# Kernel optimization log

Hardware: AMD Instinct MI355X
Metric: run time of the kernel (lower is better)

Reference implementation:

```python
import jax, jax.numpy as jnp
import numpy as np

B, T_PREFIX, C_IN = 8, 6144, 8
OUT_LEN, OUT_C = 2048, 8
AUX_DIM = 16
D_MODEL, D_STATE, HEADDIM, EXPAND = 256, 32, 64, 2
D_INNER = EXPAND * D_MODEL            # 512
NHEADS = D_INNER // HEADDIM           # 8
CONV_DIM = D_INNER + 2 * D_STATE      # 576
D_PROJ = 2 * D_INNER + 2 * D_STATE + NHEADS  # 1096
N_LAYERS = 2
CHUNK = 64
PATCH = 16
PRECONV_K = 5
DCONV_K = 4


def setup_inputs() -> dict:
    key = jax.random.key(0)
    ks = iter(jax.random.split(key, 64))
    def rn(shape, s=0.02):
        return s * jax.random.normal(next(ks), shape, jnp.float32)
    inp = dict(
        x_prefix=jax.random.normal(next(ks), (B, T_PREFIX, C_IN), jnp.float32),
        y_aux=jax.random.normal(next(ks), (B, AUX_DIM), jnp.float32),
        pre_conv_w=rn((D_MODEL, C_IN, PRECONV_K), 0.1),
        pre_conv_b=rn((D_MODEL,)),
        patch_w=rn((D_MODEL, D_MODEL, PATCH), 0.05),
        patch_b=rn((D_MODEL,)),
        mask_token=rn((D_MODEL,)),
        aux_w=rn((AUX_DIM, D_MODEL), 0.1),
        aux_b=rn((D_MODEL,)),
        patch_out_w=rn((2 * D_MODEL, OUT_C * PATCH), 0.05),
        patch_out_b=rn((OUT_C * PATCH,)),
    )
    for d in ('fwd', 'bwd'):
        inp[f'{d}_norm_w'] = jnp.ones((N_LAYERS, D_MODEL), jnp.float32)
        inp[f'{d}_inproj'] = rn((N_LAYERS, D_MODEL, D_PROJ), 0.05)
        inp[f'{d}_conv_w'] = rn((N_LAYERS, CONV_DIM, DCONV_K), 0.2)
        inp[f'{d}_conv_b'] = rn((N_LAYERS, CONV_DIM))
        inp[f'{d}_dtbias'] = rn((N_LAYERS, NHEADS), 0.5)
        inp[f'{d}_Alog'] = jnp.tile(jnp.log(jnp.arange(1, NHEADS + 1, dtype=jnp.float32)), (N_LAYERS, 1))
        inp[f'{d}_D'] = jnp.ones((N_LAYERS, NHEADS), jnp.float32)
        inp[f'{d}_gnorm'] = jnp.ones((N_LAYERS, D_INNER), jnp.float32)
        inp[f'{d}_outproj'] = rn((N_LAYERS, D_INNER, D_MODEL), 0.05)
    return inp


def rmsnorm(x, w, eps=1e-5):
    return x * jax.lax.rsqrt(jnp.mean(x * x, axis=-1, keepdims=True) + eps) * w


def conv1d(x, w, b, stride, pad):  # x: [B,C,T], w: [O,I,K]
    y = jax.lax.conv_general_dilated(x, w, (stride,), [(pad, pad)],
                                     dimension_numbers=('NCH', 'OIH', 'NCH'))
    return y + b[None, :, None]


def mamba_block(u, inproj, conv_w, conv_b, dtbias, Alog, Dp, gnorm_w, outproj):
    # Mamba-2/SSD style block: in_proj -> z | xBC | dt, causal depthwise conv,
    # selective scan with per-head scalar decay A, +D skip, gated RMSNorm, out_proj.
    b, T, _ = u.shape
    zxbcdt = u @ inproj                                   # [b,T,D_PROJ]
    z = zxbcdt[..., :D_INNER]
    xBC = zxbcdt[..., D_INNER:D_INNER + CONV_DIM]
    dt = jax.nn.softplus(zxbcdt[..., -NHEADS:] + dtbias)  # [b,T,H]
    # causal depthwise conv over time
    xc = jax.lax.conv_general_dilated(xBC.transpose(0, 2, 1), conv_w[:, None, :], (1,),
                                      [(DCONV_K - 1, 0)],
                                      dimension_numbers=('NCH', 'OIH', 'NCH'),
                                      feature_group_count=CONV_DIM)
    xBC = jax.nn.silu((xc + conv_b[None, :, None]).transpose(0, 2, 1))
    xs = xBC[..., :D_INNER].reshape(b, T, NHEADS, HEADDIM)  # [b,T,H,P]
    Bm = xBC[..., D_INNER:D_INNER + D_STATE]                # [b,T,N]
    Cm = xBC[..., D_INNER + D_STATE:]                       # [b,T,N]
    A = -jnp.exp(Alog)                                      # [H]

    def step(h, inps):  # h: [b,H,P,N]
        dt_t, x_t, B_t, C_t = inps
        dA = jnp.exp(dt_t * A)[:, :, None, None]
        h = h * dA + (dt_t[:, :, None] * x_t)[..., None] * B_t[:, None, None, :]
        y = jnp.einsum('bhpn,bn->bhp', h, C_t)
        return h, y

    h0 = jnp.zeros((b, NHEADS, HEADDIM, D_STATE), u.dtype)
    _, ys = jax.lax.scan(step, h0, (dt.transpose(1, 0, 2), xs.transpose(1, 0, 2, 3),
                                    Bm.transpose(1, 0, 2), Cm.transpose(1, 0, 2)))
    y = ys.transpose(1, 0, 2, 3) + Dp[None, None, :, None] * xs
    y = y.reshape(b, T, D_INNER)
    y = rmsnorm(y * jax.nn.silu(z), gnorm_w)
    return y @ outproj


def reference(x_prefix, y_aux, pre_conv_w, pre_conv_b, patch_w, patch_b, mask_token,
              aux_w, aux_b, fwd_norm_w, fwd_inproj, fwd_conv_w, fwd_conv_b, fwd_dtbias,
              fwd_Alog, fwd_D, fwd_gnorm, fwd_outproj, bwd_norm_w, bwd_inproj,
              bwd_conv_w, bwd_conv_b, bwd_dtbias, bwd_Alog, bwd_D, bwd_gnorm,
              bwd_outproj, patch_out_w, patch_out_b):
    b = x_prefix.shape[0]
    t_total = T_PREFIX + OUT_LEN
    x_full = jnp.pad(x_prefix, ((0, 0), (0, OUT_LEN), (0, 0)))        # zeros for future
    x = jax.nn.silu(conv1d(x_full.transpose(0, 2, 1), pre_conv_w, pre_conv_b, 1, PRECONV_K // 2))
    x = conv1d(x, patch_w, patch_b, PATCH, 0).transpose(0, 2, 1)      # [b, n_tokens, d_model]
    n_tokens = x.shape[1]
    # eval mode: deterministic future-patch mask, dropout is identity
    starts = jnp.arange(n_tokens) * PATCH
    mask = (starts >= T_PREFIX)[None, :, None]
    x = jnp.where(mask, mask_token[None, None, :], x)
    aux_bias = jax.nn.silu(y_aux @ aux_w + aux_b)[:, None, :]
    x = x + aux_bias
    pad_t = (-n_tokens) % CHUNK
    if pad_t:
        x = jnp.pad(x, ((0, 0), (0, pad_t), (0, 0)))
    h_f = x
    h_b = x[:, ::-1]
    for i in range(N_LAYERS):
        h_f = h_f + mamba_block(rmsnorm(h_f, fwd_norm_w[i]), fwd_inproj[i], fwd_conv_w[i],
                                fwd_conv_b[i], fwd_dtbias[i], fwd_Alog[i], fwd_D[i],
                                fwd_gnorm[i], fwd_outproj[i])
        h_b = h_b + mamba_block(rmsnorm(h_b, bwd_norm_w[i]), bwd_inproj[i], bwd_conv_w[i],
                                bwd_conv_b[i], bwd_dtbias[i], bwd_Alog[i], bwd_D[i],
                                bwd_gnorm[i], bwd_outproj[i])
    h = jnp.concatenate([h_f, h_b[:, ::-1]], axis=-1)[:, :n_tokens]   # [b,n,2*d_model]
    patch_pred = h @ patch_out_w + patch_out_b                        # [b,n,out_c*patch]
    y = patch_pred.reshape(b, n_tokens, OUT_C, PATCH).reshape(b, n_tokens * PATCH, OUT_C)
    y = y[:, :t_total, :]
    return y[:, T_PREFIX:, :]
```

## Files before the change

kernel.cpp:

```cpp
#include <hip/hip_runtime.h>
#include <hip/hip_bf16.h>
#include <math.h>

#define BSZ      8
#define TPREF    6144
#define CIN      8
#define DMODEL   256
#define DINNER   512
#define DSTATE   32
#define NHEADS   8
#define HEADDIM  64
#define CONVDIM  576
#define DPROJ    1096
#define NTOK     512
#define NVIS     384
#define TBWD     128
#define MFWD     (BSZ * NTOK)
#define MBWD     (BSZ * TBWD)
#define MALL     (MFWD + MBWD)

typedef float f32x4 __attribute__((ext_vector_type(4)));
typedef __bf16 bf16x8 __attribute__((ext_vector_type(8)));

__device__ __forceinline__ float silu_f(float x) { return x / (1.f + expf(-x)); }

#define ASYNC16(gp, lp) \
    __builtin_amdgcn_global_load_lds((const __attribute__((address_space(1))) void*)(gp), \
                                     (__attribute__((address_space(3))) void*)(lp), 16, 0, 0)

__global__ __launch_bounds__(256) void gemm_mfma(
    const __bf16* __restrict__ A, const __bf16* __restrict__ Bt,
    float* __restrict__ C, const float* __restrict__ bias,
    int N, int K, int ldc, int flags, long pstr) {
    __shared__ char sm[16384];
    int tid = threadIdx.x;
    int m0 = blockIdx.y * 128, n0 = blockIdx.x * 128;
    int klen = K / gridDim.z;
    int kbeg = blockIdx.z * klen;
    int w = tid >> 6, l = tid & 63;
    int wm = w >> 1, wn = w & 1;
    int lm = l & 15, q = l >> 4;

    f32x4 acc[4][4];
    #pragma unroll
    for (int i = 0; i < 4; i++)
        #pragma unroll
        for (int j = 0; j < 4; j++) acc[i][j] = (f32x4)0.f;

    for (int k0 = 0; k0 < klen; k0 += 32) {
        int kb = kbeg + k0;
        #pragma unroll
        for (int i = 0; i < 2; i++) {
            int s = i * 256 + tid;
            ASYNC16(A + (size_t)(m0 + (s >> 2)) * K + kb + (s & 3) * 8, sm + s * 16);
        }
        #pragma unroll
        for (int i = 0; i < 2; i++) {
            int s = i * 256 + tid;
            ASYNC16(Bt + (size_t)(n0 + (s >> 2)) * K + kb + (s & 3) * 8, sm + 8192 + s * 16);
        }
        __syncthreads();
        bf16x8 af[4], bfr[4];
        #pragma unroll
        for (int mf = 0; mf < 4; mf++)
            af[mf] = *(const bf16x8*)(sm + (wm * 64 + mf * 16 + lm) * 64 + q * 16);
        #pragma unroll
        for (int nf = 0; nf < 4; nf++)
            bfr[nf] = *(const bf16x8*)(sm + 8192 + (wn * 64 + nf * 16 + lm) * 64 + q * 16);
        #pragma unroll
        for (int mf = 0; mf < 4; mf++)
            #pragma unroll
            for (int nf = 0; nf < 4; nf++)
                acc[mf][nf] = __builtin_amdgcn_mfma_f32_16x16x32_bf16(af[mf], bfr[nf], acc[mf][nf], 0, 0, 0);
        __syncthreads();
    }

    #pragma unroll
    for (int mf = 0; mf < 4; mf++) {
        int mbase = m0 + wm * 64 + mf * 16 + q * 4;
        #pragma unroll
        for (int nf = 0; nf < 4; nf++) {
            int n = n0 + wn * 64 + nf * 16 + lm;
            if (n < N) {
                #pragma unroll
                for (int r = 0; r < 4; r++) {
                    float v = acc[mf][nf][r];
                    size_t ci = (size_t)(mbase + r) * ldc + n;
                    if (flags & 4) {
                        v = silu_f(v + bias[n]);
                        ((__bf16*)C)[ci] = (__bf16)v;
                    } else if (flags & 8) {
                        C[ci + (size_t)blockIdx.z * pstr] = v;
                    } else if (flags & 2) {
                        atomicAdd(C + ci, v);
                    } else {
                        C[ci] = v;
                    }
                }
            }
        }
    }
}

__global__ __launch_bounds__(256) void gemm_inproj_norm(
    const float* __restrict__ h, const float* __restrict__ wnf, const float* __restrict__ wnb,
    const __bf16* __restrict__ ipTf, const __bf16* __restrict__ ipTb,
    float* __restrict__ C) {
    __shared__ __bf16 Asm[128][264];
    __shared__ char Bsm[8192];
    int tid = threadIdx.x;
    int m0 = blockIdx.y * 128, n0 = blockIdx.x * 128;
    int dir = (m0 >= MFWD);
    const float* wnorm = dir ? wnb : wnf;
    const __bf16* Bt = dir ? ipTb : ipTf;
    {
        int row = tid >> 1, half = tid & 1;
        const float4* xr = (const float4*)(h + (size_t)(m0 + row) * 256 + half * 128);
        const float4* wr = (const float4*)(wnorm + half * 128);
        float ss = 0.f;
        #pragma unroll
        for (int c = 0; c < 32; c++) {
            float4 v = xr[c], wv = wr[c];
            ss += v.x * v.x + v.y * v.y + v.z * v.z + v.w * v.w;
            __bf16 t4b[4] = {(__bf16)(v.x * wv.x), (__bf16)(v.y * wv.y),
                             (__bf16)(v.z * wv.z), (__bf16)(v.w * wv.w)};
            *(uint2*)&Asm[row][half * 128 + c * 4] = *(uint2*)t4b;
        }
        ss += __shfl_xor(ss, 1);
        float rs = rsqrtf(ss * (1.f / 256.f) + 1e-5f);
        #pragma unroll
        for (int c = 0; c < 16; c++) {
            union { uint4 u; __bf16 hh[8]; } a;
            a.u = *(uint4*)&Asm[row][half * 128 + c * 8];
            #pragma unroll
            for (int j = 0; j < 8; j++) a.hh[j] = (__bf16)((float)a.hh[j] * rs);
            *(uint4*)&Asm[row][half * 128 + c * 8] = a.u;
        }
    }
    __syncthreads();
    int w = tid >> 6, l = tid & 63;
    int wm = w >> 1, wn_ = w & 1, lm = l & 15, q = l >> 4;
    f32x4 acc[4][4];
    #pragma unroll
    for (int i = 0; i < 4; i++)
        #pragma unroll
        for (int j = 0; j < 4; j++) acc[i][j] = (f32x4)0.f;
    for (int k0 = 0; k0 < 256; k0 += 32) {
        #pragma unroll
        for (int i = 0; i < 2; i++) {
            int s = i * 256 + tid;
            ASYNC16(Bt + (size_t)(n0 + (s >> 2)) * 256 + k0 + (s & 3) * 8, Bsm + s * 16);
        }
        __syncthreads();
        bf16x8 af[4], bfr[4];
        #pragma unroll
        for (int mf = 0; mf < 4; mf++)
            af[mf] = *(const bf16x8*)&Asm[wm * 64 + mf * 16 + lm][k0 + q * 8];
        #pragma unroll
        for (int nf = 0; nf < 4; nf++)
            bfr[nf] = *(const bf16x8*)(Bsm + (wn_ * 64 + nf * 16 + lm) * 64 + q * 16);
        #pragma unroll
        for (int mf = 0; mf < 4; mf++)
            #pragma unroll
            for (int nf = 0; nf < 4; nf++)
                acc[mf][nf] = __builtin_amdgcn_mfma_f32_16x16x32_bf16(af[mf], bfr[nf], acc[mf][nf], 0, 0, 0);
        __syncthreads();
    }
    #pragma unroll
    for (int mf = 0; mf < 4; mf++) {
        int mbase = m0 + wm * 64 + mf * 16 + q * 4;
        #pragma unroll
        for (int nf = 0; nf < 4; nf++) {
            int n = n0 + wn_ * 64 + nf * 16 + lm;
            if (n < DPROJ) {
                #pragma unroll
                for (int r = 0; r < 4; r++)
                    C[(size_t)(mbase + r) * DPROJ + n] = acc[mf][nf][r];
            }
        }
    }
}

__global__ __launch_bounds__(256) void gemm_outproj_gated(
    const __bf16* __restrict__ ysD, const float* __restrict__ zx,
    const float* __restrict__ gwf, const float* __restrict__ gwb,
    const __bf16* __restrict__ opTf, const __bf16* __restrict__ opTb,
    float* __restrict__ C) {
    __shared__ __bf16 Asm[64][520];
    __shared__ char Bsm[8192];
    int tid = threadIdx.x;
    int m0 = blockIdx.y * 64, n0 = blockIdx.x * 128;
    int dir = (m0 >= MFWD);
    const float* gw = dir ? gwb : gwf;
    const __bf16* Bt = dir ? opTb : opTf;
    {
        int row = tid >> 2, part = tid & 3;
        size_t gm = m0 + row;
        const uint4* yr = (const uint4*)(ysD + gm * 512 + part * 128);
        const float4* zr = (const float4*)(zx + gm * DPROJ + part * 128);
        const float4* gr = (const float4*)(gw + part * 128);
        float ss = 0.f;
        #pragma unroll
        for (int c = 0; c < 16; c++) {
            union { uint4 u; __bf16 hh[8]; } yv; yv.u = yr[c];
            float4 z0 = zr[c * 2], z1 = zr[c * 2 + 1];
            float4 g0 = gr[c * 2], g1 = gr[c * 2 + 1];
            float gg[8];
            gg[0] = (float)yv.hh[0] * silu_f(z0.x);
            gg[1] = (float)yv.hh[1] * silu_f(z0.y);
            gg[2] = (float)yv.hh[2] * silu_f(z0.z);
            gg[3] = (float)yv.hh[3] * silu_f(z0.w);
            gg[4] = (float)yv.hh[4] * silu_f(z1.x);
            gg[5] = (float)yv.hh[5] * silu_f(z1.y);
            gg[6] = (float)yv.hh[6] * silu_f(z1.z);
            gg[7] = (float)yv.hh[7] * silu_f(z1.w);
            #pragma unroll
            for (int j = 0; j < 8; j++) ss += gg[j] * gg[j];
            union { uint4 u; __bf16 hh[8]; } d;
            d.hh[0] = (__bf16)(gg[0] * g0.x); d.hh[1] = (__bf16)(gg[1] * g0.y);
            d.hh[2] = (__bf16)(gg[2] * g0.z); d.hh[3] = (__bf16)(gg[3] * g0.w);
            d.hh[4] = (__bf16)(gg[4] * g1.x); d.hh[5] = (__bf16)(gg[5] * g1.y);
            d.hh[6] = (__bf16)(gg[6] * g1.z); d.hh[7] = (__bf16)(gg[7] * g1.w);
            *(uint4*)&Asm[row][part * 128 + c * 8] = d.u;
        }
        ss += __shfl_xor(ss, 1);
        ss += __shfl_xor(ss, 2);
        float rs = rsqrtf(ss * (1.f / 512.f) + 1e-5f);
        #pragma unroll
        for (int c = 0; c < 16; c++) {
            union { uint4 u; __bf16 hh[8]; } a;
            a.u = *(uint4*)&Asm[row][part * 128 + c * 8];
            #pragma unroll
            for (int j = 0; j < 8; j++) a.hh[j] = (__bf16)((float)a.hh[j] * rs);
            *(uint4*)&Asm[row][part * 128 + c * 8] = a.u;
        }
    }
    __syncthreads();
    int w = tid >> 6, l = tid & 63;
    int wm = w >> 1, wn_ = w & 1, lm = l & 15, q = l >> 4;
    f32x4 acc[2][4];
    #pragma unroll
    for (int i = 0; i < 2; i++)
        #pragma unroll
        for (int j = 0; j < 4; j++) acc[i][j] = (f32x4)0.f;
    for (int k0 = 0; k0 < 512; k0 += 32) {
        #pragma unroll
        for (int i = 0; i < 2; i++) {
            int s = i * 256 + tid;
            ASYNC16(Bt + (size_t)(n0 + (s >> 2)) * 512 + k0 + (s & 3) * 8, Bsm + s * 16);
        }
        __syncthreads();
        bf16x8 af[2], bfr[4];
        #pragma unroll
        for (int mf = 0; mf < 2; mf++)
            af[mf] = *(const bf16x8*)&Asm[wm * 32 + mf * 16 + lm][k0 + q * 8];
        #pragma unroll
        for (int nf = 0; nf < 4; nf++)
            bfr[nf] = *(const bf16x8*)(Bsm + (wn_ * 64 + nf * 16 + lm) * 64 + q * 16);
        #pragma unroll
        for (int mf = 0; mf < 2; mf++)
            #pragma unroll
            for (int nf = 0; nf < 4; nf++)
                acc[mf][nf] = __builtin_amdgcn_mfma_f32_16x16x32_bf16(af[mf], bfr[nf], acc[mf][nf], 0, 0, 0);
        __syncthreads();
    }
    #pragma unroll
    for (int mf = 0; mf < 2; mf++) {
        int mbase = m0 + wm * 32 + mf * 16 + q * 4;
        #pragma unroll
        for (int nf = 0; nf < 4; nf++) {
            int n = n0 + wn_ * 64 + nf * 16 + lm;
            #pragma unroll
            for (int r = 0; r < 4; r++) {
                size_t ci = (size_t)(mbase + r) * DMODEL + n;
                C[ci] += acc[mf][nf][r];
            }
        }
    }
}

__global__ void prep_all(const float* __restrict__ pre_conv_w, const float* __restrict__ patch_w,
                         const float* __restrict__ ip0, const float* __restrict__ ip1,
                         const float* __restrict__ op0, const float* __restrict__ op1,
                         const float* __restrict__ pow_, const float* __restrict__ pob,
                         const float* __restrict__ y_aux, const float* __restrict__ aux_w,
                         const float* __restrict__ aux_b, const float* __restrict__ xp,
                         __bf16* __restrict__ WpreT, __bf16* __restrict__ WtT,
                         __bf16* __restrict__ inprojT, __bf16* __restrict__ outprojT,
                         __bf16* __restrict__ poT, float* __restrict__ auxb,
                         float* __restrict__ dout, __bf16* __restrict__ Aim) {
    __shared__ float tile[32][33];
    int bx = blockIdx.x, tid = threadIdx.x;
    int tx = tid & 31, ty = tid >> 5;
    if (bx < 256) {
        int o = bx, c = tid;
        float f[16];
        const float4* s = (const float4*)(patch_w + (size_t)o * 4096 + c * 16);
        #pragma unroll
        for (int j = 0; j < 4; j++) *(float4*)&f[j * 4] = s[j];
        #pragma unroll
        for (int k = 0; k < 16; k++)
            WtT[(size_t)o * 4096 + k * 256 + c] = (__bf16)f[k];
        return;
    }
    bx -= 256;
    if (bx < 1152) {
        int seg = bx / 288, rem = bx % 288;
        int n0 = (rem / 8) * 32, k0 = (rem % 8) * 32;
        const float* src = (seg < 2 ? ip0 : ip1) + (size_t)(seg & 1) * 256 * DPROJ;
        #pragma unroll
        for (int j = 0; j < 4; j++) {
            int r = ty + j * 8;
            int n = n0 + tx;
            tile[r][tx] = (n < DPROJ) ? src[(size_t)(k0 + r) * DPROJ + n] : 0.f;
        }
        __syncthreads();
        __bf16* dst = inprojT + (size_t)seg * 1152 * 256;
        #pragma unroll
        for (int j = 0; j < 4; j++) {
            int r = ty + j * 8;
            dst[(size_t)(n0 + r) * 256 + k0 + tx] = (__bf16)tile[tx][r];
        }
        return;
    }
    bx -= 1152;
    if (bx < 512) {
        int s = bx / 128, rem = bx % 128;
        int n0 = (rem / 16) * 32, k0 = (rem % 16) * 32;
        const float* src = (s < 2 ? op0 : op1) + (size_t)(s & 1) * DINNER * DMODEL;
        #pragma unroll
        for (int j = 0; j < 4; j++) {
            int r = ty + j * 8;
            tile[r][tx] = src[(size_t)(k0 + r) * 256 + n0 + tx];
        }
        __syncthreads();
        __bf16* dst = outprojT + (size_t)s * 256 * 512;
        #pragma unroll
        for (int j = 0; j < 4; j++) {
            int r = ty + j * 8;
            dst[(size_t)(n0 + r) * 512 + k0 + tx] = (__bf16)tile[tx][r];
        }
        return;
    }
    bx -= 512;
    if (bx < 64) {
        int n0 = (bx / 16) * 32, k0 = (bx % 16) * 32;
        #pragma unroll
        for (int j = 0; j < 4; j++) {
            int r = ty + j * 8;
            tile[r][tx] = pow_[(size_t)(k0 + r) * 128 + n0 + tx];
        }
        __syncthreads();
        #pragma unroll
        for (int j = 0; j < 4; j++) {
            int r = ty + j * 8;
            poT[(size_t)(n0 + r) * 512 + k0 + tx] = (__bf16)tile[tx][r];
        }
        return;
    }
    bx -= 64;
    if (bx < 64) {
        int idx = bx * 256 + tid;
        int o = idx >> 6, kk = idx & 63;
        WpreT[idx] = (kk < 40) ? (__bf16)pre_conv_w[o * 40 + kk] : (__bf16)0.f;
        return;
    }
    bx -= 64;
    if (bx < 512) {
        int idx = bx * 256 + tid;
        dout[idx] = pob[idx & 127];
        return;
    }
    bx -= 512;
    if (bx < 192) {
        int m = bx * 256 + tid;
        int t = m % TPREF, b = m / TPREF;
        __bf16 d[64];
        #pragma unroll
        for (int k = 0; k < 5; k++) {
            int tt = t - 2 + k;
            bool ok = (tt >= 0) && (tt < TPREF);
            const float* s = xp + ((size_t)b * TPREF + tt) * 8;
            #pragma unroll
            for (int i = 0; i < 8; i++)
                d[i * 5 + k] = ok ? (__bf16)s[i] : (__bf16)0.f;
        }
        #pragma unroll
        for (int j = 40; j < 64; j++) d[j] = (__bf16)0.f;
        uint4* o = (uint4*)(Aim + (size_t)m * 64);
        #pragma unroll
        for (int k = 0; k < 8; k++) o[k] = ((const uint4*)d)[k];
        return;
    }
    bx -= 192;
    {
        int b = bx, o = tid;
        float acc = aux_b[o];
        #pragma unroll
        for (int i = 0; i < 16; i++) acc += y_aux[b * 16 + i] * aux_w[i * 256 + o];
        auxb[b * 256 + o] = silu_f(acc);
    }
}

__global__ void assemble_kernel(const float* __restrict__ Cp4, const float* __restrict__ pb,
                                const float* __restrict__ mtok, const float* __restrict__ aux,
                                float* __restrict__ h_all) {
    int idx = blockIdx.x * 256 + threadIdx.x;
    if (idx >= BSZ * NTOK * DMODEL) return;
    int o = idx & 255, tok = (idx >> 8) & 511, b = idx >> 17;
    float v;
    if (tok < NVIS) {
        size_t ci = (size_t)(b * NVIS + tok) * 256 + o;
        v = pb[o] + Cp4[ci] + Cp4[ci + (size_t)3072 * 256] +
            Cp4[ci + (size_t)2 * 3072 * 256] + Cp4[ci + (size_t)3 * 3072 * 256];
    } else {
        v = mtok[o];
    }
    v += aux[b * 256 + o];
    h_all[idx] = v;
    if (tok >= NVIS)
        h_all[(size_t)MFWD * 256 + (size_t)(b * TBWD + (NTOK - 1 - tok)) * 256 + o] = v;
}

__global__ __launch_bounds__(256) void dwconv2_kernel(
    const float* __restrict__ zx, const float* __restrict__ cwf, const float* __restrict__ cbf,
    const float* __restrict__ cwb, const float* __restrict__ cbb,
    __bf16* __restrict__ XtF, __bf16* __restrict__ XtB,
    __bf16* __restrict__ BCF, __bf16* __restrict__ BCB) {
    int cg = blockIdx.x;
    int id = blockIdx.y;
    int b, t0, T; size_t rowbase;
    const float *cw, *cb; __bf16 *Xt, *BC;
    if (id < 64) { b = id >> 3; t0 = (id & 7) * 64; T = NTOK; rowbase = (size_t)b * NTOK;
                   cw = cwf; cb = cbf; Xt = XtF; BC = BCF; }
    else { int i2 = id - 64; b = i2 >> 1; t0 = (i2 & 1) * 64; T = TBWD;
           rowbase = (size_t)MFWD + (size_t)b * TBWD; cw = cwb; cb = cbb; Xt = XtB; BC = BCB; }
    int c0 = cg * 64;
    __shared__ float xs[67][65];
    int lane = threadIdx.x & 63, grp = threadIdx.x >> 6;
    for (int r = grp; r < 67; r += 4) {
        int t = t0 - 3 + r;
        xs[r][lane] = (t >= 0) ? zx[(rowbase + t) * DPROJ + DINNER + c0 + lane] : 0.f;
    }
    __syncthreads();
    if (cg < 8) {
        int t = lane;
        #pragma unroll
        for (int ci = grp; ci < 64; ci += 4) {
            int c = c0 + ci;
            float acc = cb[c];
            #pragma unroll
            for (int k = 0; k < 4; k++) acc += cw[c * 4 + k] * xs[t + k][ci];
            Xt[((size_t)((b * 8 + cg) * 64 + ci)) * T + t0 + t] = (__bf16)silu_f(acc);
        }
    } else {
        int c = lane;
        #pragma unroll
        for (int ti = grp; ti < 64; ti += 4) {
            float acc = cb[c0 + c];
            #pragma unroll
            for (int k = 0; k < 4; k++) acc += cw[(c0 + c) * 4 + k] * xs[ti + k][c];
            BC[((size_t)(b * T + t0 + ti)) * 64 + c] = (__bf16)silu_f(acc);
        }
    }
}

__global__ __launch_bounds__(64) void scan_local(
    const __bf16* __restrict__ XtF, const __bf16* __restrict__ XtB,
    const __bf16* __restrict__ BCF, const __bf16* __restrict__ BCB,
    const float* __restrict__ zx,
    const float* __restrict__ dtbf, const float* __restrict__ dtbb,
    const float* __restrict__ Alogf, const float* __restrict__ Alogb,
    const float* __restrict__ Dpf, const float* __restrict__ Dpb,
    __bf16* __restrict__ ysD,
    __bf16* __restrict__ ChatF, __bf16* __restrict__ ChatB,
    float* __restrict__ dSF, float* __restrict__ dSB,
    float* __restrict__ DcsF, float* __restrict__ DcsB) {
    int id = blockIdx.x, hd = blockIdx.y;
    int b, c, T, NC; size_t rowbase;
    const __bf16 *Xt, *BC; __bf16* Chat; float *dS, *Dcs;
    const float *dtb, *Alog, *Dp;
    if (id < 64) { b = id >> 3; c = id & 7; T = NTOK; NC = 8; rowbase = (size_t)b * NTOK;
                   Xt = XtF; BC = BCF; Chat = ChatF; dS = dSF; Dcs = DcsF;
                   dtb = dtbf; Alog = Alogf; Dp = Dpf; }
    else { int i2 = id - 64; b = i2 >> 1; c = i2 & 1; T = TBWD; NC = 2;
           rowbase = (size_t)MFWD + (size_t)b * TBWD;
           Xt = XtB; BC = BCB; Chat = ChatB; dS = dSB; Dcs = DcsB;
           dtb = dtbb; Alog = Alogb; Dp = Dpb; }
    int bh = b * 8 + hd;
    int t0 = c * 64;
    int lane = threadIdx.x;
    int lm = lane & 15, q = lane >> 4;
    float A = -expf(Alog[hd]);
    float Dh = Dp[hd];

    __shared__ __bf16 Xl[64][72];
    __shared__ __bf16 BCl[64][72];
    __shared__ __bf16 Pl[64][72];
    __shared__ __bf16 Wbl[32][72];
    __shared__ float lcs[64], dts[64];

    const uint4* xg = (const uint4*)(Xt + (size_t)(bh * 64 + lane) * T + t0);
    const uint4* bg = (const uint4*)(BC + ((size_t)(b * T + t0 + lane)) * 64);
    uint4 xv[8], bv[8];
    #pragma unroll
    for (int k = 0; k < 8; k++) { xv[k] = xg[k]; bv[k] = bg[k]; }
    float xdt = zx[(rowbase + t0 + lane) * DPROJ + 1088 + hd] + dtb[hd];
    float dtv = (xdt > 20.f) ? xdt : log1pf(expf(xdt));
    #pragma unroll
    for (int k = 0; k < 8; k++) {
        *(uint4*)&Xl[lane][k * 8] = xv[k];
        *(uint4*)&BCl[lane][k * 8] = bv[k];
    }
    float lc = A * dtv;
    #pragma unroll
    for (int off = 1; off < 64; off <<= 1) {
        float o = __shfl_up(lc, off);
        if (lane >= off) lc += o;
    }
    lcs[lane] = lc; dts[lane] = dtv;
    float lc63 = __shfl(lc, 63);
    float wj = expf(lc63 - lc) * dtv;
    float eli = expf(lc);
    float Dc = expf(lc63);
    if (lane == 0) Dcs[bh * NC + c] = Dc;
    {
        __bf16* co = Chat + ((size_t)(bh * NC + c) * 64 + lane) * 32;
        #pragma unroll
        for (int k = 0; k < 4; k++) {
            union { uint4 u; __bf16 h[8]; } s; s.u = bv[4 + k];
            union { uint4 u; __bf16 h[8]; } d;
            #pragma unroll
            for (int j = 0; j < 8; j++) d.h[j] = (__bf16)(eli * (float)s.h[j]);
            *(uint4*)(co + k * 8) = d.u;
        }
    }
    #pragma unroll
    for (int k = 0; k < 4; k++) {
        union { uint4 u; __bf16 h[8]; } s; s.u = bv[k];
        #pragma unroll
        for (int j = 0; j < 8; j++) Wbl[k * 8 + j][lane] = (__bf16)(wj * (float)s.h[j]);
    }
    __syncthreads();

    bf16x8 cfr[4], bfr[4];
    #pragma unroll
    for (int t4 = 0; t4 < 4; t4++) {
        cfr[t4] = *(const bf16x8*)&BCl[t4 * 16 + lm][32 + q * 8];
        bfr[t4] = *(const bf16x8*)&BCl[t4 * 16 + lm][q * 8];
    }
    #pragma unroll
    for (int ti = 0; ti < 4; ti++) {
        float lci[4];
        #pragma unroll
        for (int r = 0; r < 4; r++) lci[r] = lcs[ti * 16 + q * 4 + r];
        #pragma unroll
        for (int tj = 0; tj < 4; tj++) {
            if (tj > ti) {
                #pragma unroll
                for (int r = 0; r < 4; r++) Pl[ti * 16 + q * 4 + r][tj * 16 + lm] = (__bf16)0.f;
                continue;
            }
            f32x4 g = __builtin_amdgcn_mfma_f32_16x16x32_bf16(cfr[ti], bfr[tj], (f32x4)0.f, 0, 0, 0);
            int j = tj * 16 + lm;
            float lcj = lcs[j], dtj = dts[j];
            #pragma unroll
            for (int r = 0; r < 4; r++) {
                int i = ti * 16 + q * 4 + r;
                float v = (j <= i) ? g[r] * expf(lci[r] - lcj) * dtj : 0.f;
                if (j == i) v += Dh;
                Pl[i][j] = (__bf16)v;
            }
        }
    }
    __syncthreads();

    bf16x8 pf0[4], pf1[4], xf0[4], xf1[4];
    #pragma unroll
    for (int t4 = 0; t4 < 4; t4++) {
        pf0[t4] = *(const bf16x8*)&Pl[t4 * 16 + lm][q * 8];
        pf1[t4] = *(const bf16x8*)&Pl[t4 * 16 + lm][32 + q * 8];
        xf0[t4] = *(const bf16x8*)&Xl[t4 * 16 + lm][q * 8];
        xf1[t4] = *(const bf16x8*)&Xl[t4 * 16 + lm][32 + q * 8];
    }
    #pragma unroll
    for (int ti = 0; ti < 4; ti++) {
        #pragma unroll
        for (int tp = 0; tp < 4; tp++) {
            f32x4 y = __builtin_amdgcn_mfma_f32_16x16x32_bf16(pf0[ti], xf0[tp], (f32x4)0.f, 0, 0, 0);
            y = __builtin_amdgcn_mfma_f32_16x16x32_bf16(pf1[ti], xf1[tp], y, 0, 0, 0);
            #pragma unroll
            for (int r = 0; r < 4; r++) {
                int i = ti * 16 + q * 4 + r;
                ysD[(rowbase + t0 + i) * DINNER + hd * 64 + tp * 16 + lm] = (__bf16)y[r];
            }
        }
    }
    bf16x8 wf0[2], wf1[2];
    #pragma unroll
    for (int tn = 0; tn < 2; tn++) {
        wf0[tn] = *(const bf16x8*)&Wbl[tn * 16 + lm][q * 8];
        wf1[tn] = *(const bf16x8*)&Wbl[tn * 16 + lm][32 + q * 8];
    }
    float* dso = dS + (size_t)(bh * NC + c) * 2048;
    #pragma unroll
    for (int tp = 0; tp < 4; tp++) {
        #pragma unroll
        for (int tn = 0; tn < 2; tn++) {
            f32x4 s = __builtin_amdgcn_mfma_f32_16x16x32_bf16(xf0[tp], wf0[tn], (f32x4)0.f, 0, 0, 0);
            s = __builtin_amdgcn_mfma_f32_16x16x32_bf16(xf1[tp], wf1[tn], s, 0, 0, 0);
            #pragma unroll
            for (int r = 0; r < 4; r++) {
                int pp = tp * 16 + q * 4 + r, nn = tn * 16 + lm;
                dso[pp * 32 + nn] = s[r];
            }
        }
    }
}

__global__ __launch_bounds__(256) void scan_tail(
    const float* __restrict__ dSF, const float* __restrict__ dSB,
    const float* __restrict__ DcsF, const float* __restrict__ DcsB,
    const __bf16* __restrict__ ChatF, const __bf16* __restrict__ ChatB,
    __bf16* __restrict__ ysD) {
    int blk = blockIdx.x;
    int dir = blk >= 64;
    int bh = blk & 63;
    int NC = dir ? 2 : 8;
    int T = dir ? TBWD : NTOK;
    int b = bh >> 3, hd = bh & 7;
    size_t rowbase = dir ? ((size_t)MFWD + (size_t)b * TBWD) : ((size_t)b * NTOK);
    const float* dS = dir ? dSB : dSF;
    const float* Dcs = dir ? DcsB : DcsF;
    const __bf16* Chat = dir ? ChatB : ChatF;
    int tid = threadIdx.x;
    __shared__ __bf16 Spl[8][64][40];
    {
        int p = tid >> 2, n0 = (tid & 3) * 8;
        float S[8];
        #pragma unroll
        for (int j = 0; j < 8; j++) S[j] = 0.f;
        for (int c = 0; c < NC; c++) {
            union { uint4 u; __bf16 hh[8]; } o;
            #pragma unroll
            for (int j = 0; j < 8; j++) o.hh[j] = (__bf16)S[j];
            *(uint4*)&Spl[c][p][n0] = o.u;
            float Dc = Dcs[bh * NC + c];
            const float4* dp = (const float4*)(dS + ((size_t)(bh * NC + c)) * 2048 + tid * 8);
            float4 d0 = dp[0], d1 = dp[1];
            S[0] = Dc * S[0] + d0.x; S[1] = Dc * S[1] + d0.y;
            S[2] = Dc * S[2] + d0.z; S[3] = Dc * S[3] + d0.w;
            S[4] = Dc * S[4] + d1.x; S[5] = Dc * S[5] + d1.y;
            S[6] = Dc * S[6] + d1.z; S[7] = Dc * S[7] + d1.w;
        }
    }
    __syncthreads();
    int w = tid >> 6, l = tid & 63, lm = l & 15, q = l >> 4;
    for (int c = 1 + w; c < NC; c += 4) {
        int t0 = c * 64;
        const __bf16* Cb = Chat + (size_t)(bh * NC + c) * 2048;
        bf16x8 cf[4], sf[4];
        #pragma unroll
        for (int t4 = 0; t4 < 4; t4++) {
            cf[t4] = *(const bf16x8*)(Cb + (t4 * 16 + lm) * 32 + q * 8);
            sf[t4] = *(const bf16x8*)&Spl[c][t4 * 16 + lm][q * 8];
        }
        #pragma unroll
        for (int ti = 0; ti < 4; ti++) {
            #pragma unroll
            for (int tp = 0; tp < 4; tp++) {
                f32x4 y = __builtin_amdgcn_mfma_f32_16x16x32_bf16(cf[ti], sf[tp], (f32x4)0.f, 0, 0, 0);
                #pragma unroll
                for (int r = 0; r < 4; r++) {
                    int i = ti * 16 + q * 4 + r;
                    size_t idx = (rowbase + t0 + i) * DINNER + hd * 64 + tp * 16 + lm;
                    ysD[idx] = (__bf16)((float)ysD[idx] + y[r]);
                }
            }
        }
    }
}

__global__ void hcat_kernel(const float* __restrict__ h_all, __bf16* __restrict__ hc) {
    int idx = blockIdx.x * 256 + threadIdx.x;
    if (idx >= BSZ * TBWD * DINNER) return;
    int c = idx & 511, j = (idx >> 9) & 127, b = idx >> 16;
    float v = (c < 256) ? h_all[(size_t)(b * NTOK + NVIS + j) * 256 + c]
                        : h_all[(size_t)MFWD * 256 + (size_t)(b * TBWD + (TBWD - 1 - j)) * 256 + (c - 256)];
    hc[idx] = (__bf16)v;
}

extern "C" void kernel_launch(void* const* d_in, const int* in_sizes, int n_in,
                              void* d_out, int out_size, void* d_ws, size_t ws_size,
                              hipStream_t stream) {
    const float* x_prefix    = (const float*)d_in[0];
    const float* y_aux       = (const float*)d_in[1];
    const float* pre_conv_w  = (const float*)d_in[2];
    const float* pre_conv_b  = (const float*)d_in[3];
    const float* patch_w     = (const float*)d_in[4];
    const float* patch_b     = (const float*)d_in[5];
    const float* mask_token  = (const float*)d_in[6];
    const float* aux_w       = (const float*)d_in[7];
    const float* aux_b       = (const float*)d_in[8];
    const float* patch_out_w = (const float*)d_in[9];
    const float* patch_out_b = (const float*)d_in[10];
    const float* w_norm[2]   = {(const float*)d_in[11], (const float*)d_in[20]};
    const float* w_inproj[2] = {(const float*)d_in[12], (const float*)d_in[21]};
    const float* w_convw[2]  = {(const float*)d_in[13], (const float*)d_in[22]};
    const float* w_convb[2]  = {(const float*)d_in[14], (const float*)d_in[23]};
    const float* w_dtb[2]    = {(const float*)d_in[15], (const float*)d_in[24]};
    const float* w_alog[2]   = {(const float*)d_in[16], (const float*)d_in[25]};
    const float* w_D[2]      = {(const float*)d_in[17], (const float*)d_in[26]};
    const float* w_gnorm[2]  = {(const float*)d_in[18], (const float*)d_in[27]};
    const float* w_outproj[2]= {(const float*)d_in[19], (const float*)d_in[28]};

    char* p = (char*)d_ws;
    auto alloc = [&](size_t bytes) { char* r = p; p += (bytes + 255) & ~255ULL; return r; };
    __bf16* A_patch  = (__bf16*)alloc((size_t)3072 * 4096 * 2);
    __bf16* Aim      = (__bf16*)alloc((size_t)BSZ * TPREF * 64 * 2);
    __bf16* WpreT    = (__bf16*)alloc((size_t)256 * 64 * 2);
    __bf16* WtT      = (__bf16*)alloc((size_t)256 * 4096 * 2);
    __bf16* inprojT  = (__bf16*)alloc((size_t)4 * 1152 * 256 * 2);
    __bf16* outprojT = (__bf16*)alloc((size_t)4 * 256 * 512 * 2);
    __bf16* poT      = (__bf16*)alloc((size_t)128 * 512 * 2);
    float*  auxb     = (float*)alloc(8 * 256 * 4);
    float*  Cp4      = (float*)alloc((size_t)4 * 3072 * 256 * 4);
    float*  h_all    = (float*)alloc((size_t)MALL * 256 * 4);
    float*  zx       = (float*)alloc((size_t)MALL * DPROJ * 4);
    __bf16* XtF      = (__bf16*)alloc((size_t)64 * 64 * NTOK * 2);
    __bf16* XtB      = (__bf16*)alloc((size_t)64 * 64 * TBWD * 2);
    __bf16* BCF      = (__bf16*)alloc((size_t)BSZ * NTOK * 64 * 2);
    __bf16* BCB      = (__bf16*)alloc((size_t)BSZ * TBWD * 64 * 2);
    __bf16* ysD      = (__bf16*)alloc((size_t)MALL * DINNER * 2);
    __bf16* hct      = (__bf16*)alloc((size_t)1024 * DINNER * 2);
    __bf16* ChatF    = (__bf16*)alloc((size_t)64 * 8 * 2048 * 2);
    __bf16* ChatB    = (__bf16*)alloc((size_t)64 * 2 * 2048 * 2);
    float*  dSF      = (float*)alloc((size_t)64 * 8 * 2048 * 4);
    float*  dSB      = (float*)alloc((size_t)64 * 2 * 2048 * 4);
    float*  DcsF     = (float*)alloc((size_t)64 * 8 * 4);
    float*  DcsB     = (float*)alloc((size_t)64 * 2 * 4);

    prep_all<<<256 + 1152 + 512 + 64 + 64 + 512 + 192 + 8, 256, 0, stream>>>(
        pre_conv_w, patch_w, w_inproj[0], w_inproj[1], w_outproj[0], w_outproj[1],
        patch_out_w, patch_out_b, y_aux, aux_w, aux_b, x_prefix,
        WpreT, WtT, inprojT, outprojT, poT, auxb, (float*)d_out, Aim);
    gemm_mfma<<<dim3(2, (BSZ * TPREF) / 128, 1), 256, 0, stream>>>(
        Aim, WpreT, (float*)A_patch, pre_conv_b, 256, 64, 256, 4, 0);
    gemm_mfma<<<dim3(2, 24, 4), 256, 0, stream>>>(
        A_patch, WtT, Cp4, nullptr, 256, 4096, 256, 8, (long)3072 * 256);
    assemble_kernel<<<(BSZ * NTOK * DMODEL) / 256, 256, 0, stream>>>(
        Cp4, patch_b, mask_token, auxb, h_all);

    for (int i = 0; i < 2; i++) {
        const __bf16* ipTf = inprojT + (size_t)(0 * 2 + i) * 1152 * 256;
        const __bf16* ipTb = inprojT + (size_t)(1 * 2 + i) * 1152 * 256;
        const __bf16* opTf = outprojT + (size_t)(0 * 2 + i) * 256 * 512;
        const __bf16* opTb = outprojT + (size_t)(1 * 2 + i) * 256 * 512;
        gemm_inproj_norm<<<dim3(9, MALL / 128), 256, 0, stream>>>(
            h_all, w_norm[0] + i * 256, w_norm[1] + i * 256, ipTf, ipTb, zx);
        dwconv2_kernel<<<dim3(9, 80), 256, 0, stream>>>(
            zx, w_convw[0] + i * CONVDIM * 4, w_convb[0] + i * CONVDIM,
            w_convw[1] + i * CONVDIM * 4, w_convb[1] + i * CONVDIM,
            XtF, XtB, BCF, BCB);
        scan_local<<<dim3(80, NHEADS), 64, 0, stream>>>(
            XtF, XtB, BCF, BCB, zx,
            w_dtb[0] + i * 8, w_dtb[1] + i * 8,
            w_alog[0] + i * 8, w_alog[1] + i * 8,
            w_D[0] + i * 8, w_D[1] + i * 8,
            ysD, ChatF, ChatB, dSF, dSB, DcsF, DcsB);
        scan_tail<<<128, 256, 0, stream>>>(dSF, dSB, DcsF, DcsB, ChatF, ChatB, ysD);
        gemm_outproj_gated<<<dim3(2, MALL / 64), 256, 0, stream>>>(
            ysD, zx, w_gnorm[0] + i * DINNER, w_gnorm[1] + i * DINNER, opTf, opTb, h_all);
    }

    hcat_kernel<<<(BSZ * TBWD * DINNER) / 256, 256, 0, stream>>>(h_all, hct);
    gemm_mfma<<<dim3(1, 8, 4), 256, 0, stream>>>(
        hct, poT, (float*)d_out, nullptr, 128, 512, 128, 2, 0);
}
```

Baseline: 381.1 us.

## Skip unneeded last-layer forward outputs, fuse hcat into final GEMM, widen patch split-K

After: 446.9 us. 1.17x slower.

```diff
diff --git a/kernel.cpp b/kernel.cpp
--- a/kernel.cpp
+++ b/kernel.cpp
@@ -102,6 +102,72 @@
     }
 }
 
+__global__ __launch_bounds__(256) void final_gemm(
+    const float* __restrict__ h_all, const __bf16* __restrict__ poT,
+    float* __restrict__ out) {
+    __shared__ __bf16 Asm_[128][40];
+    __shared__ char Bsm[8192];
+    int tid = threadIdx.x;
+    int m0 = blockIdx.y * 128;
+    int z = blockIdx.z;
+    int w = tid >> 6, l = tid & 63;
+    int wm = w >> 1, wn_ = w & 1, lm = l & 15, q = l >> 4;
+    f32x4 acc[4][4];
+    #pragma unroll
+    for (int i = 0; i < 4; i++)
+        #pragma unroll
+        for (int j = 0; j < 4; j++) acc[i][j] = (f32x4)0.f;
+
+    int r = tid >> 1, half = tid & 1;
+    int m = m0 + r;
+    int b = m >> 7, jj = m & 127;
+    size_t arow = (z == 0) ? ((size_t)(b * NTOK + NVIS + jj) * 256)
+                           : ((size_t)MFWD * 256 + (size_t)(b * TBWD + (TBWD - 1 - jj)) * 256);
+    for (int k0 = 0; k0 < 256; k0 += 32) {
+        {
+            const float4* sp = (const float4*)(h_all + arow + k0 + half * 16);
+            float4 v0 = sp[0], v1 = sp[1], v2 = sp[2], v3 = sp[3];
+            union { uint4 u; __bf16 hh[8]; } d0, d1;
+            d0.hh[0] = (__bf16)v0.x; d0.hh[1] = (__bf16)v0.y; d0.hh[2] = (__bf16)v0.z; d0.hh[3] = (__bf16)v0.w;
+            d0.hh[4] = (__bf16)v1.x; d0.hh[5] = (__bf16)v1.y; d0.hh[6] = (__bf16)v1.z; d0.hh[7] = (__bf16)v1.w;
+            d1.hh[0] = (__bf16)v2.x; d1.hh[1] = (__bf16)v2.y; d1.hh[2] = (__bf16)v2.z; d1.hh[3] = (__bf16)v2.w;
+            d1.hh[4] = (__bf16)v3.x; d1.hh[5] = (__bf16)v3.y; d1.hh[6] = (__bf16)v3.z; d1.hh[7] = (__bf16)v3.w;
+            *(uint4*)&Asm_[r][half * 16] = d0.u;
+            *(uint4*)&Asm_[r][half * 16 + 8] = d1.u;
+        }
+        #pragma unroll
+        for (int i = 0; i < 2; i++) {
+            int s = i * 256 + tid;
+            ASYNC16(poT + (size_t)(s >> 2) * 512 + z * 256 + k0 + (s & 3) * 8, Bsm + s * 16);
+        }
+        __syncthreads();
+        bf16x8 af[4], bfr[4];
+        #pragma unroll
+        for (int mf = 0; mf < 4; mf++)
+            af[mf] = *(const bf16x8*)&Asm_[wm * 64 + mf * 16 + lm][q * 8];
+        #pragma unroll
+        for (int nf = 0; nf < 4; nf++)
+            bfr[nf] = *(const bf16x8*)(Bsm + (wn_ * 64 + nf * 16 + lm) * 64 + q * 16);
+        #pragma unroll
+        for (int mf = 0; mf < 4; mf++)
+            #pragma unroll
+            for (int nf = 0; nf < 4; nf++)
+                acc[mf][nf] = __builtin_amdgcn_mfma_f32_16x16x32_bf16(af[mf], bfr[nf], acc[mf][nf], 0, 0, 0);
+        __syncthreads();
+    }
+    #pragma unroll
+    for (int mf = 0; mf < 4; mf++) {
+        int mbase = m0 + wm * 64 + mf * 16 + q * 4;
+        #pragma unroll
+        for (int nf = 0; nf < 4; nf++) {
+            int n = wn_ * 64 + nf * 16 + lm;
+            #pragma unroll
+            for (int rr = 0; rr < 4; rr++)
+                atomicAdd(out + (size_t)(mbase + rr) * 128 + n, acc[mf][nf][rr]);
+        }
+    }
+}
+
 __global__ __launch_bounds__(256) void gemm_inproj_norm(
     const float* __restrict__ h, const float* __restrict__ wnf, const float* __restrict__ wnb,
     const __bf16* __restrict__ ipTf, const __bf16* __restrict__ ipTb,
@@ -185,11 +251,15 @@
     const __bf16* __restrict__ ysD, const float* __restrict__ zx,
     const float* __restrict__ gwf, const float* __restrict__ gwb,
     const __bf16* __restrict__ opTf, const __bf16* __restrict__ opTb,
-    float* __restrict__ C) {
+    float* __restrict__ C, int layer) {
     __shared__ __bf16 Asm[64][520];
     __shared__ char Bsm[8192];
     int tid = threadIdx.x;
-    int m0 = blockIdx.y * 64, n0 = blockIdx.x * 128;
+    int yb = blockIdx.y;
+    int m0;
+    if (layer == 0) m0 = yb * 64;
+    else m0 = (yb < 16) ? ((yb >> 1) * 512 + 384 + (yb & 1) * 64) : (MFWD + (yb - 16) * 64);
+    int n0 = blockIdx.x * 128;
     int dir = (m0 >= MFWD);
     const float* gw = dir ? gwb : gwf;
     const __bf16* Bt = dir ? opTb : opTf;
@@ -402,7 +472,7 @@
     }
 }
 
-__global__ void assemble_kernel(const float* __restrict__ Cp4, const float* __restrict__ pb,
+__global__ void assemble_kernel(const float* __restrict__ Cp8, const float* __restrict__ pb,
                                 const float* __restrict__ mtok, const float* __restrict__ aux,
                                 float* __restrict__ h_all) {
     int idx = blockIdx.x * 256 + threadIdx.x;
@@ -411,8 +481,9 @@
     float v;
     if (tok < NVIS) {
         size_t ci = (size_t)(b * NVIS + tok) * 256 + o;
-        v = pb[o] + Cp4[ci] + Cp4[ci + (size_t)3072 * 256] +
-            Cp4[ci + (size_t)2 * 3072 * 256] + Cp4[ci + (size_t)3 * 3072 * 256];
+        v = pb[o];
+        #pragma unroll
+        for (int z = 0; z < 8; z++) v += Cp8[ci + (size_t)z * 3072 * 256];
     } else {
         v = mtok[o];
     }
@@ -475,7 +546,7 @@
     __bf16* __restrict__ ysD,
     __bf16* __restrict__ ChatF, __bf16* __restrict__ ChatB,
     float* __restrict__ dSF, float* __restrict__ dSB,
-    float* __restrict__ DcsF, float* __restrict__ DcsB) {
+    float* __restrict__ DcsF, float* __restrict__ DcsB, int layer) {
     int id = blockIdx.x, hd = blockIdx.y;
     int b, c, T, NC; size_t rowbase;
     const __bf16 *Xt, *BC; __bf16* Chat; float *dS, *Dcs;
@@ -487,6 +558,7 @@
            rowbase = (size_t)MFWD + (size_t)b * TBWD;
            Xt = XtB; BC = BCB; Chat = ChatB; dS = dSB; Dcs = DcsB;
            dtb = dtbb; Alog = Alogb; Dp = Dpb; }
+    bool skipY = (layer == 1) && (id < 64) && (c < 6);
     int bh = b * 8 + hd;
     int t0 = c * 64;
     int lane = threadIdx.x;
@@ -494,11 +566,13 @@
     float A = -expf(Alog[hd]);
     float Dh = Dp[hd];
 
-    __shared__ __bf16 Xl[64][72];
-    __shared__ __bf16 BCl[64][72];
-    __shared__ __bf16 Pl[64][72];
-    __shared__ __bf16 Wbl[32][72];
-    __shared__ float lcs[64], dts[64];
+    __shared__ char smem[23552];
+    __bf16 (*Xl)[72]  = (__bf16(*)[72])(smem);
+    __bf16 (*BCl)[72] = (__bf16(*)[72])(smem + 9216);
+    __bf16 (*Pl)[72]  = (__bf16(*)[72])(smem + 9216);
+    __bf16 (*Wbl)[72] = (__bf16(*)[72])(smem + 18432);
+    float* lcs = (float*)(smem + 23040);
+    float* dts = (float*)(smem + 23296);
 
     const uint4* xg = (const uint4*)(Xt + (size_t)(bh * 64 + lane) * T + t0);
     const uint4* bg = (const uint4*)(BC + ((size_t)(b * T + t0 + lane)) * 64);
@@ -510,7 +584,7 @@
     #pragma unroll
     for (int k = 0; k < 8; k++) {
         *(uint4*)&Xl[lane][k * 8] = xv[k];
-        *(uint4*)&BCl[lane][k * 8] = bv[k];
+        if (!skipY) *(uint4*)&BCl[lane][k * 8] = bv[k];
     }
     float lc = A * dtv;
     #pragma unroll
@@ -524,7 +598,7 @@
     float eli = expf(lc);
     float Dc = expf(lc63);
     if (lane == 0) Dcs[bh * NC + c] = Dc;
-    {
+    if (!skipY) {
         __bf16* co = Chat + ((size_t)(bh * NC + c) * 64 + lane) * 32;
         #pragma unroll
         for (int k = 0; k < 4; k++) {
@@ -543,57 +617,66 @@
     }
     __syncthreads();
 
-    bf16x8 cfr[4], bfr[4];
-    #pragma unroll
-    for (int t4 = 0; t4 < 4; t4++) {
-        cfr[t4] = *(const bf16x8*)&BCl[t4 * 16 + lm][32 + q * 8];
-        bfr[t4] = *(const bf16x8*)&BCl[t4 * 16 + lm][q * 8];
-    }
-    #pragma unroll
-    for (int ti = 0; ti < 4; ti++) {
-        float lci[4];
-        #pragma unroll
-        for (int r = 0; r < 4; r++) lci[r] = lcs[ti * 16 + q * 4 + r];
-        #pragma unroll
-        for (int tj = 0; tj < 4; tj++) {
-            if (tj > ti) {
+    bf16x8 xf0[4], xf1[4];
+    if (!skipY) {
+        bf16x8 cfr[4], bfr[4];
+        #pragma unroll
+        for (int t4 = 0; t4 < 4; t4++) {
+            cfr[t4] = *(const bf16x8*)&BCl[t4 * 16 + lm][32 + q * 8];
+            bfr[t4] = *(const bf16x8*)&BCl[t4 * 16 + lm][q * 8];
+        }
+        #pragma unroll
+        for (int ti = 0; ti < 4; ti++) {
+            float lci[4];
+            #pragma unroll
+            for (int r = 0; r < 4; r++) lci[r] = lcs[ti * 16 + q * 4 + r];
+            #pragma unroll
+            for (int tj = 0; tj < 4; tj++) {
+                if (tj > ti) {
+                    #pragma unroll
+                    for (int r = 0; r < 4; r++) Pl[ti * 16 + q * 4 + r][tj * 16 + lm] = (__bf16)0.f;
+                    continue;
+                }
+                f32x4 g = __builtin_amdgcn_mfma_f32_16x16x32_bf16(cfr[ti], bfr[tj], (f32x4)0.f, 0, 0, 0);
+                int j = tj * 16 + lm;
+                float lcj = lcs[j], dtj = dts[j];
                 #pragma unroll
-                for (int r = 0; r < 4; r++) Pl[ti * 16 + q * 4 + r][tj * 16 + lm] = (__bf16)0.f;
-                continue;
+                for (int r = 0; r < 4; r++) {
+                    int i = ti * 16 + q * 4 + r;
+                    float v = (j <= i) ? g[r] * expf(lci[r] - lcj) * dtj : 0.f;
+                    if (j == i) v += Dh;
+                    Pl[i][j] = (__bf16)v;
+                }
             }
-            f32x4 g = __builtin_amdgcn_mfma_f32_16x16x32_bf16(cfr[ti], bfr[tj], (f32x4)0.f, 0, 0, 0);
-            int j = tj * 16 + lm;
-            float lcj = lcs[j], dtj = dts[j];
-            #pragma unroll
-            for (int r = 0; r < 4; r++) {
-                int i = ti * 16 + q * 4 + r;
-                float v = (j <= i) ? g[r] * expf(lci[r] - lcj) * dtj : 0.f;
-                if (j == i) v += Dh;
-                Pl[i][j] = (__bf16)v;
+        }
+        __syncthreads();
+
+        bf16x8 pf0[4], pf1[4];
+        #pragma unroll
+        for (int t4 = 0; t4 < 4; t4++) {
+            pf0[t4] = *(const bf16x8*)&Pl[t4 * 16 + lm][q * 8];
+            pf1[t4] = *(const bf16x8*)&Pl[t4 * 16 + lm][32 + q * 8];
+            xf0[t4] = *(const bf16x8*)&Xl[t4 * 16 + lm][q * 8];
+            xf1[t4] = *(const bf16x8*)&Xl[t4 * 16 + lm][32 + q * 8];
+        }
+        #pragma unroll
+        for (int ti = 0; ti < 4; ti++) {
+            #pragma unroll
+            for (int tp = 0; tp < 4; tp++) {
+                f32x4 y = __builtin_amdgcn_mfma_f32_16x16x32_bf16(pf0[ti], xf0[tp], (f32x4)0.f, 0, 0, 0);
+                y = __builtin_amdgcn_mfma_f32_16x16x32_bf16(pf1[ti], xf1[tp], y, 0, 0, 0);
+                #pragma unroll
+                for (int r = 0; r < 4; r++) {
+                    int i = ti * 16 + q * 4 + r;
+                    ysD[(rowbase + t0 + i) * DINNER + hd * 64 + tp * 16 + lm] = (__bf16)y[r];
+                }
             }
         }
-    }
-    __syncthreads();
-
-    bf16x8 pf0[4], pf1[4], xf0[4], xf1[4];
-    #pragma unroll
-    for (int t4 = 0; t4 < 4; t4++) {
-        pf0[t4] = *(const bf16x8*)&Pl[t4 * 16 + lm][q * 8];
-        pf1[t4] = *(const bf16x8*)&Pl[t4 * 16 + lm][32 + q * 8];
-        xf0[t4] = *(const bf16x8*)&Xl[t4 * 16 + lm][q * 8];
-        xf1[t4] = *(const bf16x8*)&Xl[t4 * 16 + lm][32 + q * 8];
-    }
-    #pragma unroll
-    for (int ti = 0; ti < 4; ti++) {
-        #pragma unroll
-        for (int tp = 0; tp < 4; tp++) {
-            f32x4 y = __builtin_amdgcn_mfma_f32_16x16x32_bf16(pf0[ti], xf0[tp], (f32x4)0.f, 0, 0, 0);
-            y = __builtin_amdgcn_mfma_f32_16x16x32_bf16(pf1[ti], xf1[tp], y, 0, 0, 0);
-            #pragma unroll
-            for (int r = 0; r < 4; r++) {
-                int i = ti * 16 + q * 4 + r;
-                ysD[(rowbase + t0 + i) * DINNER + hd * 64 + tp * 16 + lm] = (__bf16)y[r];
-            }
+    } else {
+        #pragma unroll
+        for (int t4 = 0; t4 < 4; t4++) {
+            xf0[t4] = *(const bf16x8*)&Xl[t4 * 16 + lm][q * 8];
+            xf1[t4] = *(const bf16x8*)&Xl[t4 * 16 + lm][32 + q * 8];
         }
     }
     bf16x8 wf0[2], wf1[2];
@@ -622,7 +705,7 @@
     const float* __restrict__ dSF, const float* __restrict__ dSB,
     const float* __restrict__ DcsF, const float* __restrict__ DcsB,
     const __bf16* __restrict__ ChatF, const __bf16* __restrict__ ChatB,
-    __bf16* __restrict__ ysD) {
+    __bf16* __restrict__ ysD, int layer) {
     int blk = blockIdx.x;
     int dir = blk >= 64;
     int bh = blk & 63;
@@ -633,6 +716,7 @@
     const float* dS = dir ? dSB : dSF;
     const float* Dcs = dir ? DcsB : DcsF;
     const __bf16* Chat = dir ? ChatB : ChatF;
+    int cmin = (layer == 1 && !dir) ? 6 : 1;
     int tid = threadIdx.x;
     __shared__ __bf16 Spl[8][64][40];
     {
@@ -656,7 +740,7 @@
     }
     __syncthreads();
     int w = tid >> 6, l = tid & 63, lm = l & 15, q = l >> 4;
-    for (int c = 1 + w; c < NC; c += 4) {
+    for (int c = cmin + w; c < NC; c += 4) {
         int t0 = c * 64;
         const __bf16* Cb = Chat + (size_t)(bh * NC + c) * 2048;
         bf16x8 cf[4], sf[4];
@@ -679,15 +763,6 @@
             }
         }
     }
-}
-
-__global__ void hcat_kernel(const float* __restrict__ h_all, __bf16* __restrict__ hc) {
-    int idx = blockIdx.x * 256 + threadIdx.x;
-    if (idx >= BSZ * TBWD * DINNER) return;
-    int c = idx & 511, j = (idx >> 9) & 127, b = idx >> 16;
-    float v = (c < 256) ? h_all[(size_t)(b * NTOK + NVIS + j) * 256 + c]
-                        : h_all[(size_t)MFWD * 256 + (size_t)(b * TBWD + (TBWD - 1 - j)) * 256 + (c - 256)];
-    hc[idx] = (__bf16)v;
 }
 
 extern "C" void kernel_launch(void* const* d_in, const int* in_sizes, int n_in,
@@ -724,7 +799,7 @@
     __bf16* outprojT = (__bf16*)alloc((size_t)4 * 256 * 512 * 2);
     __bf16* poT      = (__bf16*)alloc((size_t)128 * 512 * 2);
     float*  auxb     = (float*)alloc(8 * 256 * 4);
-    float*  Cp4      = (float*)alloc((size_t)4 * 3072 * 256 * 4);
+    float*  Cp8      = (float*)alloc((size_t)8 * 3072 * 256 * 4);
     float*  h_all    = (float*)alloc((size_t)MALL * 256 * 4);
     float*  zx       = (float*)alloc((size_t)MALL * DPROJ * 4);
     __bf16* XtF      = (__bf16*)alloc((size_t)64 * 64 * NTOK * 2);
@@ -732,7 +807,6 @@
     __bf16* BCF      = (__bf16*)alloc((size_t)BSZ * NTOK * 64 * 2);
     __bf16* BCB      = (__bf16*)alloc((size_t)BSZ * TBWD * 64 * 2);
     __bf16* ysD      = (__bf16*)alloc((size_t)MALL * DINNER * 2);
-    __bf16* hct      = (__bf16*)alloc((size_t)1024 * DINNER * 2);
     __bf16* ChatF    = (__bf16*)alloc((size_t)64 * 8 * 2048 * 2);
     __bf16* ChatB    = (__bf16*)alloc((size_t)64 * 2 * 2048 * 2);
     float*  dSF      = (float*)alloc((size_t)64 * 8 * 2048 * 4);
@@ -746,10 +820,10 @@
         WpreT, WtT, inprojT, outprojT, poT, auxb, (float*)d_out, Aim);
     gemm_mfma<<<dim3(2, (BSZ * TPREF) / 128, 1), 256, 0, stream>>>(
         Aim, WpreT, (float*)A_patch, pre_conv_b, 256, 64, 256, 4, 0);
-    gemm_mfma<<<dim3(2, 24, 4), 256, 0, stream>>>(
-        A_patch, WtT, Cp4, nullptr, 256, 4096, 256, 8, (long)3072 * 256);
+    gemm_mfma<<<dim3(2, 24, 8), 256, 0, stream>>>(
+        A_patch, WtT, Cp8, nullptr, 256, 4096, 256, 8, (long)3072 * 256);
     assemble_kernel<<<(BSZ * NTOK * DMODEL) / 256, 256, 0, stream>>>(
-        Cp4, patch_b, mask_token, auxb, h_all);
+        Cp8, patch_b, mask_token, auxb, h_all);
 
     for (int i = 0; i < 2; i++) {
         const __bf16* ipTf = inprojT + (size_t)(0 * 2 + i) * 1152 * 256;
@@ -767,13 +841,12 @@
             w_dtb[0] + i * 8, w_dtb[1] + i * 8,
             w_alog[0] + i * 8, w_alog[1] + i * 8,
             w_D[0] + i * 8, w_D[1] + i * 8,
-            ysD, ChatF, ChatB, dSF, dSB, DcsF, DcsB);
-        scan_tail<<<128, 256, 0, stream>>>(dSF, dSB, DcsF, DcsB, ChatF, ChatB, ysD);
-        gemm_outproj_gated<<<dim3(2, MALL / 64), 256, 0, stream>>>(
-            ysD, zx, w_gnorm[0] + i * DINNER, w_gnorm[1] + i * DINNER, opTf, opTb, h_all);
-    }
-
-    hcat_kernel<<<(BSZ * TBWD * DINNER) / 256, 256, 0, stream>>>(h_all, hct);
-    gemm_mfma<<<dim3(1, 8, 4), 256, 0, stream>>>(
-        hct, poT, (float*)d_out, nullptr, 128, 512, 128, 2, 0);
-}
+            ysD, ChatF, ChatB, dSF, dSB, DcsF, DcsB, i);
+        scan_tail<<<128, 256, 0, stream>>>(dSF, dSB, DcsF, DcsB, ChatF, ChatB, ysD, i);
+        int oy = (i == 0) ? (MALL / 64) : 32;
+        gemm_outproj_gated<<<dim3(2, oy), 256, 0, stream>>>(
+            ysD, zx, w_gnorm[0] + i * DINNER, w_gnorm[1] + i * DINNER, opTf, opTb, h_all, i);
+    }
+
+    final_gemm<<<dim3(1, 8, 2), 256, 0, stream>>>(h_all, poT, (float*)d_out);
+}
```
